# Kernel tuning notes

Measured on AMD Instinct MI355X. Metric: run time of the kernel, lower is better.

## Reference

```python
import jax, jax.numpy as jnp
import numpy as np

N, E, F, H, B = 100000, 3200000, 128, 32, 256
NEG_SLOPE = 0.2  # PyG GATv2Conv default negative_slope


def setup_inputs() -> dict:
    key = jax.random.key(0)
    ks = jax.random.split(key, 8)
    x = jax.random.normal(ks[0], (N, F), jnp.float32)
    edge_index = jax.random.randint(ks[1], (2, E), 0, N, dtype=jnp.int32)
    # sorted graph ids covering all B graphs (PyG batch vector is sorted)
    batch = (jnp.arange(N, dtype=jnp.int32) * B) // N
    init = lambda k, shape, fan: (jax.random.normal(k, shape, jnp.float32) / np.float32(np.sqrt(fan)))
    Wl = init(ks[2], (F, H), F)
    Wr = init(ks[3], (F, H), F)
    att = init(ks[4], (H,), H)
    bias = jnp.zeros((H,), jnp.float32)
    W1 = init(ks[5], (H, 1024), H); b1 = jnp.zeros((1024,), jnp.float32)
    W2 = init(ks[6], (1024, 512), 1024); b2 = jnp.zeros((512,), jnp.float32)
    W3 = init(ks[7], (512, 4), 512); b3 = jnp.zeros((4,), jnp.float32)
    return dict(x=x, edge_index=edge_index, batch=batch, Wl=Wl, Wr=Wr,
                att=att, bias=bias, W1=W1, b1=b1, W2=W2, b2=b2, W3=W3, b3=b3)


def reference(x, edge_index, batch, Wl, Wr, att, bias, W1, b1, W2, b2, W3, b3):
    # ---- GATv2Conv (single head, sum aggregation, self-loops added) ----
    loop = jnp.arange(N, dtype=edge_index.dtype)
    src = jnp.concatenate([edge_index[0], loop])  # [E+N] message sources
    dst = jnp.concatenate([edge_index[1], loop])  # [E+N] message targets
    xl = x @ Wl  # [N,H] source-side transform
    xr = x @ Wr  # [N,H] target-side transform
    # GATv2 score: a^T LeakyReLU(Wl x_src + Wr x_dst)
    e = jax.nn.leaky_relu(xl[src] + xr[dst], NEG_SLOPE) @ att  # [E+N]
    # segment softmax over incoming edges of each target node
    m = jax.ops.segment_max(e, dst, num_segments=N)  # every node has a self-loop
    p = jnp.exp(e - m[dst])
    z = jax.ops.segment_sum(p, dst, num_segments=N)
    alpha = p / z[dst]  # [E+N]
    node_out = jax.ops.segment_sum(alpha[:, None] * xl[src], dst, num_segments=N) + bias  # [N,H]
    # ---- global max pool over each graph ----
    g = jax.ops.segment_max(node_out, batch, num_segments=B)  # [B,H]
    # ---- classification MLP head ----
    h = jax.nn.relu(g @ W1 + b1)
    h = jax.nn.relu(h @ W2 + b2)
    return h @ W3 + b3  # [B,4]
```

## Files before the change

### kernel.cpp

```cpp
#include <hip/hip_runtime.h>
#include <hip/hip_fp16.h>

#define N_NODES 100000
#define N_EDGES 3200000
#define F_IN    128
#define H_DIM   32
#define B_GR    256
#define NEG     0.2f

#define FBIN_SZ  100
#define N_FBIN   (N_NODES / FBIN_SZ)
#define BIN_CAP  4096
#define CPAD     16
#define PART_T   1024
#define EPB_R    8
#define EPB_G    (PART_T * EPB_R)
#define PART_NBLK ((N_EDGES / 4 + EPB_G - 1) / EPB_G)
#define LIN_BLK  ((N_NODES + 63) / 64)

__device__ __forceinline__ unsigned fenc(float f) {
    unsigned u = __float_as_uint(f);
    return (u & 0x80000000u) ? ~u : (u | 0x80000000u);
}
__device__ __forceinline__ float fdec(unsigned u) {
    return (u & 0x80000000u) ? __uint_as_float(u & 0x7FFFFFFFu)
                             : __uint_as_float(~u);
}

__global__ __launch_bounds__(1024) void k_fused(
    const int* __restrict__ ei, int* __restrict__ bcnt, unsigned* __restrict__ binbuf,
    const float* __restrict__ x, const float* __restrict__ Wl,
    const float* __restrict__ Wr, __half* __restrict__ xl16, float* __restrict__ xr)
{
    __shared__ __align__(16) float smem[16384];
    int t = threadIdx.x;

    if (blockIdx.x < PART_NBLK) {
        int* lcnt = (int*)smem;
        int* cur  = lcnt + 1024;
        lcnt[t] = 0;
        __syncthreads();
        int g0 = blockIdx.x * EPB_G;
        const int4* dsrc = (const int4*)(ei + N_EDGES);
        const int4* ssrc = (const int4*)ei;
        #pragma unroll
        for (int r = 0; r < EPB_R; ++r) {
            int i = g0 + r * PART_T + t;
            if (i < N_EDGES / 4) {
                int4 d = dsrc[i];
                atomicAdd(&lcnt[d.x / FBIN_SZ], 1);
                atomicAdd(&lcnt[d.y / FBIN_SZ], 1);
                atomicAdd(&lcnt[d.z / FBIN_SZ], 1);
                atomicAdd(&lcnt[d.w / FBIN_SZ], 1);
            }
        }
        __syncthreads();
        if (t < N_FBIN) {
            int c = lcnt[t];
            if (c > 0) cur[t] = atomicAdd(&bcnt[t * CPAD], c);
        }
        __syncthreads();
        #pragma unroll
        for (int r = 0; r < EPB_R; ++r) {
            int i = g0 + r * PART_T + t;
            if (i < N_EDGES / 4) {
                int4 s = ssrc[i];
                int4 d = dsrc[i];
                int b, p;
                b = d.x / FBIN_SZ; p = atomicAdd(&cur[b], 1);
                binbuf[(size_t)b * BIN_CAP + p] = ((unsigned)(d.x - b * FBIN_SZ) << 17) | (unsigned)s.x;
                b = d.y / FBIN_SZ; p = atomicAdd(&cur[b], 1);
                binbuf[(size_t)b * BIN_CAP + p] = ((unsigned)(d.y - b * FBIN_SZ) << 17) | (unsigned)s.y;
                b = d.z / FBIN_SZ; p = atomicAdd(&cur[b], 1);
                binbuf[(size_t)b * BIN_CAP + p] = ((unsigned)(d.z - b * FBIN_SZ) << 17) | (unsigned)s.z;
                b = d.w / FBIN_SZ; p = atomicAdd(&cur[b], 1);
                binbuf[(size_t)b * BIN_CAP + p] = ((unsigned)(d.w - b * FBIN_SZ) << 17) | (unsigned)s.w;
            }
        }
    } else {
        float* Wls = smem;
        float* Wrs = smem + 4096;
        float* xsb = smem + 8192;
        int blk = blockIdx.x - PART_NBLK;
        for (int i = t; i < F_IN * H_DIM; i += 1024) { Wls[i] = Wl[i]; Wrs[i] = Wr[i]; }
        int q = t >> 8, tq = t & 255;
        size_t base = (size_t)blk * 64 + q * 16;
        bool act = base < N_NODES;
        float* xs = xsb + q * 2048;
        if (act) {
            const float4* xg = (const float4*)(x + base * F_IN);
            float4* xs4 = (float4*)xs;
            xs4[tq] = xg[tq];
            xs4[tq + 256] = xg[tq + 256];
        }
        __syncthreads();
        if (act) {
            int nl = tq >> 5, h = tq & 31;
            float al0 = 0.f, ar0 = 0.f, al1 = 0.f, ar1 = 0.f;
            const float4* xa4 = (const float4*)(xs + nl * F_IN);
            const float4* xb4 = (const float4*)(xs + (nl + 8) * F_IN);
            #pragma unroll 8
            for (int f4 = 0; f4 < 32; ++f4) {
                float4 xa = xa4[f4], xb = xb4[f4];
                int fb = f4 * 4;
                float w;
                w = Wls[(fb + 0) * 32 + h]; al0 = fmaf(xa.x, w, al0); al1 = fmaf(xb.x, w, al1);
                w = Wls[(fb + 1) * 32 + h]; al0 = fmaf(xa.y, w, al0); al1 = fmaf(xb.y, w, al1);
                w = Wls[(fb + 2) * 32 + h]; al0 = fmaf(xa.z, w, al0); al1 = fmaf(xb.z, w, al1);
                w = Wls[(fb + 3) * 32 + h]; al0 = fmaf(xa.w, w, al0); al1 = fmaf(xb.w, w, al1);
                w = Wrs[(fb + 0) * 32 + h]; ar0 = fmaf(xa.x, w, ar0); ar1 = fmaf(xb.x, w, ar1);
                w = Wrs[(fb + 1) * 32 + h]; ar0 = fmaf(xa.y, w, ar0); ar1 = fmaf(xb.y, w, ar1);
                w = Wrs[(fb + 2) * 32 + h]; ar0 = fmaf(xa.z, w, ar0); ar1 = fmaf(xb.z, w, ar1);
                w = Wrs[(fb + 3) * 32 + h]; ar0 = fmaf(xa.w, w, ar0); ar1 = fmaf(xb.w, w, ar1);
            }
            size_t n0 = base + nl, n1 = base + nl + 8;
            xl16[n0 * 32 + h] = __float2half(al0); xr[n0 * 32 + h] = ar0;
            xl16[n1 * 32 + h] = __float2half(al1); xr[n1 * 32 + h] = ar1;
        }
    }
}

__global__ __launch_bounds__(512) void k_aggregate(
    const unsigned* __restrict__ binbuf, const int* __restrict__ bcnt,
    const __half* __restrict__ xl16, const float* __restrict__ xr,
    const float* __restrict__ att, const float* __restrict__ bias,
    const int* __restrict__ batch, unsigned* __restrict__ gu)
{
    __shared__ unsigned eL[BIN_CAP];
    __shared__ int cnt[128];
    __shared__ int sc[128];
    __shared__ int cur[128];
    __shared__ unsigned lmax[64];
    int t = threadIdx.x;
    int bin = blockIdx.x;
    int n_e = bcnt[bin * CPAD];
    const unsigned* bb = binbuf + (size_t)bin * BIN_CAP;

    if (t < 128) cnt[t] = 0;
    if (t < 64) lmax[t] = 0u;
    __syncthreads();
    for (int i = t; i < n_e; i += 512)
        atomicAdd(&cnt[bb[i] >> 17], 1);
    __syncthreads();
    if (t < 128) sc[t] = cnt[t];
    __syncthreads();
    for (int off = 1; off < 128; off <<= 1) {
        int v = 0;
        if (t < 128 && t >= off) v = sc[t - off];
        __syncthreads();
        if (t < 128) sc[t] += v;
        __syncthreads();
    }
    if (t < 128) cur[t] = sc[t] - cnt[t];
    __syncthreads();
    for (int i = t; i < n_e; i += 512) {
        unsigned u = bb[i];
        int p = atomicAdd(&cur[u >> 17], 1);
        eL[p] = u;
    }
    __syncthreads();

    int lane = t & 63;
    int wv = t >> 6;
    int half = lane >> 5;
    int gid = (lane >> 4) & 1;
    int hp = lane & 15;
    const float2 a2 = ((const float2*)att)[hp];
    const float2 b2 = ((const float2*)bias)[hp];
    int lg0 = batch[bin * FBIN_SZ];

    for (int nl = wv * 2 + half; nl < FBIN_SZ; nl += 16) {
        int n = bin * FBIN_SZ + nl;
        int e0 = (nl > 0) ? sc[nl - 1] : 0;
        int e1 = sc[nl];
        const float2 xr2 = ((const float2*)(xr + (size_t)n * H_DIM))[hp];
        const float2 xl2 = __half22float2(((const __half2*)(xl16 + (size_t)n * H_DIM))[hp]);

        float vx = xl2.x + xr2.x; vx = fmaxf(vx, vx * NEG);
        float vy = xl2.y + xr2.y; vy = fmaxf(vy, vy * NEG);
        float pr = vx * a2.x; pr = fmaf(vy, a2.y, pr);
        pr += __shfl_xor(pr, 1); pr += __shfl_xor(pr, 2);
        pr += __shfl_xor(pr, 4); pr += __shfl_xor(pr, 8);
        float z = 0.f; float2 acc = make_float2(0.f, 0.f);
        if (gid == 0) {
            float p = __expf(fminf(pr, 70.f));
            z = p; acc.x = p * xl2.x; acc.y = p * xl2.y;
        }

        int j = e0 + gid;
        for (; j + 2 < e1; j += 4) {
            unsigned uA = eL[j], uB = eL[j + 2];
            int sA = (int)(uA & 0x1FFFFu), sB = (int)(uB & 0x1FFFFu);
            float2 xA = __half22float2(((const __half2*)(xl16 + (size_t)sA * H_DIM))[hp]);
            float2 xB = __half22float2(((const __half2*)(xl16 + (size_t)sB * H_DIM))[hp]);
            float ax = xA.x + xr2.x; ax = fmaxf(ax, ax * NEG);
            float ay = xA.y + xr2.y; ay = fmaxf(ay, ay * NEG);
            float bx = xB.x + xr2.x; bx = fmaxf(bx, bx * NEG);
            float by = xB.y + xr2.y; by = fmaxf(by, by * NEG);
            float pA = ax * a2.x; pA = fmaf(ay, a2.y, pA);
            float pB = bx * a2.x; pB = fmaf(by, a2.y, pB);
            pA += __shfl_xor(pA, 1); pB += __shfl_xor(pB, 1);
            pA += __shfl_xor(pA, 2); pB += __shfl_xor(pB, 2);
            pA += __shfl_xor(pA, 4); pB += __shfl_xor(pB, 4);
            pA += __shfl_xor(pA, 8); pB += __shfl_xor(pB, 8);
            float eA = __expf(fminf(pA, 70.f));
            float eB = __expf(fminf(pB, 70.f));
            z += eA + eB;
            acc.x = fmaf(eA, xA.x, acc.x); acc.y = fmaf(eA, xA.y, acc.y);
            acc.x = fmaf(eB, xB.x, acc.x); acc.y = fmaf(eB, xB.y, acc.y);
        }
        for (; j < e1; j += 2) {
            unsigned u = eL[j];
            int s = (int)(u & 0x1FFFFu);
            float2 xs2 = __half22float2(((const __half2*)(xl16 + (size_t)s * H_DIM))[hp]);
            float ex = xs2.x + xr2.x; ex = fmaxf(ex, ex * NEG);
            float ey = xs2.y + xr2.y; ey = fmaxf(ey, ey * NEG);
            float pp = ex * a2.x; pp = fmaf(ey, a2.y, pp);
            pp += __shfl_xor(pp, 1); pp += __shfl_xor(pp, 2);
            pp += __shfl_xor(pp, 4); pp += __shfl_xor(pp, 8);
            float p = __expf(fminf(pp, 70.f));
            z += p;
            acc.x = fmaf(p, xs2.x, acc.x);
            acc.y = fmaf(p, xs2.y, acc.y);
        }

        z += __shfl_xor(z, 16);
        acc.x += __shfl_xor(acc.x, 16);
        acc.y += __shfl_xor(acc.y, 16);

        if (gid == 0) {
            float inv = 1.f / z;
            float ox = fmaf(acc.x, inv, b2.x);
            float oy = fmaf(acc.y, inv, b2.y);
            int gi = batch[n] - lg0;
            atomicMax(&lmax[gi * 32 + hp * 2 + 0], fenc(ox));
            atomicMax(&lmax[gi * 32 + hp * 2 + 1], fenc(oy));
        }
    }
    __syncthreads();
    if (t < 64) {
        int g = lg0 + (t >> 5);
        int glast = batch[bin * FBIN_SZ + FBIN_SZ - 1];
        if (g <= glast) atomicMax(&gu[g * H_DIM + (t & 31)], lmax[t]);
    }
}

__global__ __launch_bounds__(512) void k_head(
    const unsigned* __restrict__ gu, const float* __restrict__ W1,
    const float* __restrict__ b1, const float* __restrict__ W2,
    const float* __restrict__ b2, const float* __restrict__ W3,
    const float* __restrict__ b3, float* __restrict__ out)
{
    __shared__ float gs[H_DIM];
    __shared__ float h1s[1024];
    __shared__ float h2s[512];
    int b = blockIdx.x, t = threadIdx.x;
    if (t < H_DIM) gs[t] = fdec(gu[b * H_DIM + t]);
    __syncthreads();
    #pragma unroll
    for (int jj = 0; jj < 2; ++jj) {
        int j = jj * 512 + t;
        float a = b1[j];
        #pragma unroll
        for (int k = 0; k < H_DIM; ++k) a = fmaf(gs[k], W1[k * 1024 + j], a);
        h1s[j] = fmaxf(a, 0.f);
    }
    __syncthreads();
    {
        float a0 = 0.f, a1 = 0.f, a2 = 0.f, a3 = 0.f;
        #pragma unroll 4
        for (int k = 0; k < 256; ++k) {
            a0 = fmaf(h1s[k      ], W2[(size_t)(k      ) * 512 + t], a0);
            a1 = fmaf(h1s[k + 256], W2[(size_t)(k + 256) * 512 + t], a1);
            a2 = fmaf(h1s[k + 512], W2[(size_t)(k + 512) * 512 + t], a2);
            a3 = fmaf(h1s[k + 768], W2[(size_t)(k + 768) * 512 + t], a3);
        }
        h2s[t] = fmaxf((a0 + a1) + (a2 + a3) + b2[t], 0.f);
    }
    __syncthreads();
    if (t < 256) {
        int c = t >> 6, lane = t & 63;
        float a = 0.f;
        #pragma unroll
        for (int k = lane; k < 512; k += 64)
            a = fmaf(h2s[k], W3[k * 4 + c], a);
        for (int off = 32; off; off >>= 1) a += __shfl_down(a, off);
        if (lane == 0) out[b * 4 + c] = a + b3[c];
    }
}

extern "C" void kernel_launch(void* const* d_in, const int* in_sizes, int n_in,
                              void* d_out, int out_size, void* d_ws, size_t ws_size,
                              hipStream_t stream)
{
    const float* x     = (const float*)d_in[0];
    const int*   ei    = (const int*)d_in[1];
    const int*   batch = (const int*)d_in[2];
    const float* Wl    = (const float*)d_in[3];
    const float* Wr    = (const float*)d_in[4];
    const float* att   = (const float*)d_in[5];
    const float* bias  = (const float*)d_in[6];
    const float* W1    = (const float*)d_in[7];
    const float* b1    = (const float*)d_in[8];
    const float* W2    = (const float*)d_in[9];
    const float* b2    = (const float*)d_in[10];
    const float* W3    = (const float*)d_in[11];
    const float* b3    = (const float*)d_in[12];
    float* out = (float*)d_out;

    __half*   xl16   = (__half*)d_ws;
    float*    xr     = (float*)(xl16 + (size_t)N_NODES * H_DIM);
    unsigned* binbuf = (unsigned*)(xr + (size_t)N_NODES * H_DIM);
    int*      bcnt   = (int*)(binbuf + (size_t)N_FBIN * BIN_CAP);
    unsigned* gu     = (unsigned*)(bcnt + N_FBIN * CPAD);

    hipMemsetAsync(bcnt, 0, (size_t)(N_FBIN * CPAD + B_GR * H_DIM) * sizeof(int), stream);

    k_fused<<<PART_NBLK + LIN_BLK, 1024, 0, stream>>>(
        ei, bcnt, binbuf, x, Wl, Wr, xl16, xr);
    k_aggregate<<<N_FBIN, 512, 0, stream>>>(binbuf, bcnt, xl16, xr, att, bias, batch, gu);
    k_head<<<B_GR, 512, 0, stream>>>(gu, W1, b1, W2, b2, W3, b3, out);
}
```

Before: 169.3 us.

## Process four nodes per wavefront with 8-lane float4 feature slices

Remaps lanes in the per-node aggregation so each 16-lane group handles one node, using 8 lanes of 4 features each (one 8-byte half load per lane) instead of 16 lanes of 2 features. This cuts the shuffle reduction by one step and doubles nodes in flight per wave. It also grows the node bin size to 125 with a larger bin capacity, so there are fewer blocks, each doing more work. The risks are higher register use and possible overflow of the bin buffer for high-degree bins.

Result: faster. 156.5 us (-7.5%).

```diff
diff --git a/kernel.cpp b/kernel.cpp
--- a/kernel.cpp
+++ b/kernel.cpp
@@ -8,9 +8,9 @@
 #define B_GR    256
 #define NEG     0.2f
 
-#define FBIN_SZ  100
+#define FBIN_SZ  125
 #define N_FBIN   (N_NODES / FBIN_SZ)
-#define BIN_CAP  4096
+#define BIN_CAP  5120
 #define CPAD     16
 #define PART_T   1024
 #define EPB_R    8
@@ -162,79 +162,116 @@
 
     int lane = t & 63;
     int wv = t >> 6;
-    int half = lane >> 5;
-    int gid = (lane >> 4) & 1;
-    int hp = lane & 15;
-    const float2 a2 = ((const float2*)att)[hp];
-    const float2 b2 = ((const float2*)bias)[hp];
+    int ns = (lane >> 4) & 3;
+    int stream = (lane >> 3) & 1;
+    int oct = lane & 7;
+    const float4 a4 = ((const float4*)att)[oct];
+    const float4 b4 = ((const float4*)bias)[oct];
     int lg0 = batch[bin * FBIN_SZ];
 
-    for (int nl = wv * 2 + half; nl < FBIN_SZ; nl += 16) {
+    for (int nl = wv * 4 + ns; nl < FBIN_SZ; nl += 32) {
         int n = bin * FBIN_SZ + nl;
         int e0 = (nl > 0) ? sc[nl - 1] : 0;
         int e1 = sc[nl];
-        const float2 xr2 = ((const float2*)(xr + (size_t)n * H_DIM))[hp];
-        const float2 xl2 = __half22float2(((const __half2*)(xl16 + (size_t)n * H_DIM))[hp]);
-
-        float vx = xl2.x + xr2.x; vx = fmaxf(vx, vx * NEG);
-        float vy = xl2.y + xr2.y; vy = fmaxf(vy, vy * NEG);
-        float pr = vx * a2.x; pr = fmaf(vy, a2.y, pr);
-        pr += __shfl_xor(pr, 1); pr += __shfl_xor(pr, 2);
-        pr += __shfl_xor(pr, 4); pr += __shfl_xor(pr, 8);
-        float z = 0.f; float2 acc = make_float2(0.f, 0.f);
-        if (gid == 0) {
-            float p = __expf(fminf(pr, 70.f));
-            z = p; acc.x = p * xl2.x; acc.y = p * xl2.y;
-        }
-
-        int j = e0 + gid;
+        const float4 xr4 = ((const float4*)(xr + (size_t)n * H_DIM))[oct];
+        float2 raw = ((const float2*)(xl16 + (size_t)n * H_DIM))[oct];
+        float2 sf0 = __half22float2(*(__half2*)&raw.x);
+        float2 sf1 = __half22float2(*(__half2*)&raw.y);
+
+        float z = 0.f;
+        float4 acc = make_float4(0.f, 0.f, 0.f, 0.f);
+        {
+            float vx = sf0.x + xr4.x; vx = fmaxf(vx, vx * NEG);
+            float vy = sf0.y + xr4.y; vy = fmaxf(vy, vy * NEG);
+            float vz = sf1.x + xr4.z; vz = fmaxf(vz, vz * NEG);
+            float vw = sf1.y + xr4.w; vw = fmaxf(vw, vw * NEG);
+            float pr = vx * a4.x;
+            pr = fmaf(vy, a4.y, pr);
+            pr = fmaf(vz, a4.z, pr);
+            pr = fmaf(vw, a4.w, pr);
+            pr += __shfl_xor(pr, 1);
+            pr += __shfl_xor(pr, 2);
+            pr += __shfl_xor(pr, 4);
+            if (stream == 0) {
+                float p = __expf(fminf(pr, 70.f));
+                z = p;
+                acc = make_float4(p * sf0.x, p * sf0.y, p * sf1.x, p * sf1.y);
+            }
+        }
+
+        int j = e0 + stream;
         for (; j + 2 < e1; j += 4) {
             unsigned uA = eL[j], uB = eL[j + 2];
             int sA = (int)(uA & 0x1FFFFu), sB = (int)(uB & 0x1FFFFu);
-            float2 xA = __half22float2(((const __half2*)(xl16 + (size_t)sA * H_DIM))[hp]);
-            float2 xB = __half22float2(((const __half2*)(xl16 + (size_t)sB * H_DIM))[hp]);
-            float ax = xA.x + xr2.x; ax = fmaxf(ax, ax * NEG);
-            float ay = xA.y + xr2.y; ay = fmaxf(ay, ay * NEG);
-            float bx = xB.x + xr2.x; bx = fmaxf(bx, bx * NEG);
-            float by = xB.y + xr2.y; by = fmaxf(by, by * NEG);
-            float pA = ax * a2.x; pA = fmaf(ay, a2.y, pA);
-            float pB = bx * a2.x; pB = fmaf(by, a2.y, pB);
+            float2 rA = ((const float2*)(xl16 + (size_t)sA * H_DIM))[oct];
+            float2 rB = ((const float2*)(xl16 + (size_t)sB * H_DIM))[oct];
+            float2 A0 = __half22float2(*(__half2*)&rA.x);
+            float2 A1 = __half22float2(*(__half2*)&rA.y);
+            float2 B0 = __half22float2(*(__half2*)&rB.x);
+            float2 B1 = __half22float2(*(__half2*)&rB.y);
+            float pA, pB;
+            {
+                float vx = A0.x + xr4.x; vx = fmaxf(vx, vx * NEG);
+                float vy = A0.y + xr4.y; vy = fmaxf(vy, vy * NEG);
+                float vz = A1.x + xr4.z; vz = fmaxf(vz, vz * NEG);
+                float vw = A1.y + xr4.w; vw = fmaxf(vw, vw * NEG);
+                pA = vx * a4.x; pA = fmaf(vy, a4.y, pA);
+                pA = fmaf(vz, a4.z, pA); pA = fmaf(vw, a4.w, pA);
+            }
+            {
+                float vx = B0.x + xr4.x; vx = fmaxf(vx, vx * NEG);
+                float vy = B0.y + xr4.y; vy = fmaxf(vy, vy * NEG);
+                float vz = B1.x + xr4.z; vz = fmaxf(vz, vz * NEG);
+                float vw = B1.y + xr4.w; vw = fmaxf(vw, vw * NEG);
+                pB = vx * a4.x; pB = fmaf(vy, a4.y, pB);
+                pB = fmaf(vz, a4.z, pB); pB = fmaf(vw, a4.w, pB);
+            }
             pA += __shfl_xor(pA, 1); pB += __shfl_xor(pB, 1);
             pA += __shfl_xor(pA, 2); pB += __shfl_xor(pB, 2);
             pA += __shfl_xor(pA, 4); pB += __shfl_xor(pB, 4);
-            pA += __shfl_xor(pA, 8); pB += __shfl_xor(pB, 8);
             float eA = __expf(fminf(pA, 70.f));
             float eB = __expf(fminf(pB, 70.f));
             z += eA + eB;
-            acc.x = fmaf(eA, xA.x, acc.x); acc.y = fmaf(eA, xA.y, acc.y);
-            acc.x = fmaf(eB, xB.x, acc.x); acc.y = fmaf(eB, xB.y, acc.y);
+            acc.x = fmaf(eA, A0.x, acc.x); acc.y = fmaf(eA, A0.y, acc.y);
+            acc.z = fmaf(eA, A1.x, acc.z); acc.w = fmaf(eA, A1.y, acc.w);
+            acc.x = fmaf(eB, B0.x, acc.x); acc.y = fmaf(eB, B0.y, acc.y);
+            acc.z = fmaf(eB, B1.x, acc.z); acc.w = fmaf(eB, B1.y, acc.w);
         }
         for (; j < e1; j += 2) {
             unsigned u = eL[j];
             int s = (int)(u & 0x1FFFFu);
-            float2 xs2 = __half22float2(((const __half2*)(xl16 + (size_t)s * H_DIM))[hp]);
-            float ex = xs2.x + xr2.x; ex = fmaxf(ex, ex * NEG);
-            float ey = xs2.y + xr2.y; ey = fmaxf(ey, ey * NEG);
-            float pp = ex * a2.x; pp = fmaf(ey, a2.y, pp);
-            pp += __shfl_xor(pp, 1); pp += __shfl_xor(pp, 2);
-            pp += __shfl_xor(pp, 4); pp += __shfl_xor(pp, 8);
+            float2 rS = ((const float2*)(xl16 + (size_t)s * H_DIM))[oct];
+            float2 S0 = __half22float2(*(__half2*)&rS.x);
+            float2 S1 = __half22float2(*(__half2*)&rS.y);
+            float vx = S0.x + xr4.x; vx = fmaxf(vx, vx * NEG);
+            float vy = S0.y + xr4.y; vy = fmaxf(vy, vy * NEG);
+            float vz = S1.x + xr4.z; vz = fmaxf(vz, vz * NEG);
+            float vw = S1.y + xr4.w; vw = fmaxf(vw, vw * NEG);
+            float pp = vx * a4.x; pp = fmaf(vy, a4.y, pp);
+            pp = fmaf(vz, a4.z, pp); pp = fmaf(vw, a4.w, pp);
+            pp += __shfl_xor(pp, 1);
+            pp += __shfl_xor(pp, 2);
+            pp += __shfl_xor(pp, 4);
             float p = __expf(fminf(pp, 70.f));
             z += p;
-            acc.x = fmaf(p, xs2.x, acc.x);
-            acc.y = fmaf(p, xs2.y, acc.y);
-        }
-
-        z += __shfl_xor(z, 16);
-        acc.x += __shfl_xor(acc.x, 16);
-        acc.y += __shfl_xor(acc.y, 16);
-
-        if (gid == 0) {
+            acc.x = fmaf(p, S0.x, acc.x); acc.y = fmaf(p, S0.y, acc.y);
+            acc.z = fmaf(p, S1.x, acc.z); acc.w = fmaf(p, S1.y, acc.w);
+        }
+
+        z += __shfl_xor(z, 8);
+        acc.x += __shfl_xor(acc.x, 8);
+        acc.y += __shfl_xor(acc.y, 8);
+        acc.z += __shfl_xor(acc.z, 8);
+        acc.w += __shfl_xor(acc.w, 8);
+
+        if (stream == 0) {
             float inv = 1.f / z;
-            float ox = fmaf(acc.x, inv, b2.x);
-            float oy = fmaf(acc.y, inv, b2.y);
             int gi = batch[n] - lg0;
-            atomicMax(&lmax[gi * 32 + hp * 2 + 0], fenc(ox));
-            atomicMax(&lmax[gi * 32 + hp * 2 + 1], fenc(oy));
+            int base = gi * 32 + oct * 4;
+            atomicMax(&lmax[base + 0], fenc(fmaf(acc.x, inv, b4.x)));
+            atomicMax(&lmax[base + 1], fenc(fmaf(acc.y, inv, b4.y)));
+            atomicMax(&lmax[base + 2], fenc(fmaf(acc.z, inv, b4.z)));
+            atomicMax(&lmax[base + 3], fenc(fmaf(acc.w, inv, b4.w)));
         }
     }
     __syncthreads();
```
